# Kernel tuning notes

Hardware: AMD Instinct MI355X
Metric: run time of the kernel (lower is better)

Reference implementation:

```python
import jax, jax.numpy as jnp
import numpy as np

# SemiConv2d with semifield_type='MaxMin':
#   out[n,oc,i,j] = max_{ic,kh,kw} min(x_pad[n,ic,i+kh,j+kw], kernel[oc,ic,kh,kw])
# stride=1, 'same' padding with -inf (identity of max).

def setup_inputs() -> dict:
    key = jax.random.key(0)
    kx, kk = jax.random.split(key)
    x = jax.random.normal(kx, (8, 32, 96, 96), dtype=jnp.float32)
    kernel = jax.random.normal(kk, (32, 32, 3, 3), dtype=jnp.float32)
    return {"x": x, "kernel": kernel}


def reference(x, kernel):
    N, IC, H, W = x.shape
    OC, IC2, KH, KW = kernel.shape
    assert IC == IC2
    # same padding for k=3, stride=1 (left=top=1, right=bottom=1)
    p = KH - 1
    top = left = p // 2
    bot = right = p - top
    xp = jnp.pad(x, ((0, 0), (0, 0), (top, bot), (left, right)),
                 constant_values=-jnp.inf)
    out = None
    # small fixed loop over kernel taps (KH*KW = 9); vectorized over N, OC, IC, H, W
    for kh in range(KH):
        for kw in range(KW):
            win = xp[:, :, kh:kh + H, kw:kw + W]           # [N, IC, H, W]
            k_tap = kernel[:, :, kh, kw]                   # [OC, IC]
            # min over values, max over input channels -> [N, OC, H, W]
            v = jnp.max(jnp.minimum(win[:, None], k_tap[None, :, :, None, None]), axis=2)
            out = v if out is None else jnp.maximum(out, v)
    return out
```

## Files before the change

### kernel.cpp

```cpp
#include <hip/hip_runtime.h>
#include <math.h>


#define HH 96
#define WW 96
#define CIN 32
#define OCN 32
#define XQ_ROWS 98
#define XQ_W 48
#define XQ_SLICE (XQ_ROWS * XQ_W)
#define XQ_TOTAL (256 * XQ_SLICE)
#define K2_TOTAL (8 * 32 * 4 * 9)
#define WS_NEED ((size_t)XQ_TOTAL * 8 + (size_t)K2_TOTAL * 4)
#define NEGH2 0xFC00FC00u

typedef _Float16 h2 __attribute__((ext_vector_type(2)));

__device__ __forceinline__ uint32_t pkmin_vs(uint32_t x, uint32_t k) {
    uint32_t d;
    asm("v_pk_min_f16 %0, %1, %2" : "=v"(d) : "v"(x), "s"(k));
    return d;
}
__device__ __forceinline__ uint32_t pkmax(uint32_t a, uint32_t b) {
    uint32_t d;
    asm("v_pk_max_f16 %0, %1, %2" : "=v"(d) : "v"(a), "v"(b));
    return d;
}

__global__ __launch_bounds__(256) void setup_xq(const float* __restrict__ x,
                                                uint2* __restrict__ xq) {
    int idx = blockIdx.x * 256 + threadIdx.x;
    int j  = idx % XQ_W;
    int t  = idx / XQ_W;
    int hp = t % XQ_ROWS;
    int s  = t / XQ_ROWS;
    int h  = hp - 1;
    bool hv = (h >= 0) && (h < HH);
    const float* row = x + ((size_t)s * HH + (hv ? h : 0)) * WW;
    float a = (hv && j > 0)        ? row[2 * j - 1] : -INFINITY;
    float b = hv                   ? row[2 * j]     : -INFINITY;
    float c = hv                   ? row[2 * j + 1] : -INFINITY;
    float d = (hv && j < XQ_W - 1) ? row[2 * j + 2] : -INFINITY;
    h2 p0 = {(_Float16)a, (_Float16)b};
    h2 p1 = {(_Float16)c, (_Float16)d};
    uint2 v;
    v.x = __builtin_bit_cast(uint32_t, p0);
    v.y = __builtin_bit_cast(uint32_t, p1);
    xq[idx] = v;
}

__global__ __launch_bounds__(256) void setup_k(const float* __restrict__ kk,
                                               uint32_t* __restrict__ k2) {
    int idx = blockIdx.x * 256 + threadIdx.x;
    int tap  = idx % 9;
    int ocin = (idx / 9) % 4;
    int ic   = (idx / 36) % CIN;
    int ocb  = idx / (36 * CIN);
    float v = kk[(((ocb * 4 + ocin) * CIN) + ic) * 9 + tap];
    _Float16 hv = (_Float16)v;
    h2 p = {hv, hv};
    k2[idx] = __builtin_bit_cast(uint32_t, p);
}

__global__ __launch_bounds__(192) void semiconv_f16(const uint2* __restrict__ xq,
                                                    const uint32_t* __restrict__ k2,
                                                    float* __restrict__ out) {
    const int tid = threadIdx.x;
    const int jj = tid % 48;
    const int hr = tid / 48;
    const int b  = blockIdx.x;
    const int hp  = b % 24;
    const int t   = b / 24;
    const int ocb = t & 7;
    const int n   = t >> 3;
    const int h   = hp * 4 + hr;

    const uint2* p = xq + ((size_t)(n * CIN) * XQ_ROWS + h) * XQ_W + jj;
    const uint32_t* kp = k2 + (size_t)ocb * CIN * 36;

    uint32_t acc[4] = {NEGH2, NEGH2, NEGH2, NEGH2};

    for (int ic0 = 0; ic0 < CIN; ic0 += 2) {
        uint2 q[2][3];
#pragma unroll
        for (int u = 0; u < 2; ++u)
#pragma unroll
            for (int r = 0; r < 3; ++r)
                q[u][r] = p[u * XQ_SLICE + r * XQ_W];

#pragma unroll
        for (int u = 0; u < 2; ++u) {
            uint32_t tap[9];
#pragma unroll
            for (int r = 0; r < 3; ++r) {
                tap[r * 3 + 0] = q[u][r].x;
                tap[r * 3 + 1] = __builtin_amdgcn_alignbit(q[u][r].y, q[u][r].x, 16);
                tap[r * 3 + 2] = q[u][r].y;
            }
            const uint32_t* kq0 = kp + (ic0 + u) * 36;
#pragma unroll
            for (int oc = 0; oc < 4; ++oc) {
                const uint32_t* kq = kq0 + oc * 9;
                uint32_t m0 = pkmin_vs(tap[0], kq[0]);
                uint32_t m1 = pkmin_vs(tap[1], kq[1]);
                uint32_t m2 = pkmin_vs(tap[2], kq[2]);
                uint32_t m3 = pkmin_vs(tap[3], kq[3]);
                uint32_t m4 = pkmin_vs(tap[4], kq[4]);
                uint32_t m5 = pkmin_vs(tap[5], kq[5]);
                uint32_t m6 = pkmin_vs(tap[6], kq[6]);
                uint32_t m7 = pkmin_vs(tap[7], kq[7]);
                uint32_t m8 = pkmin_vs(tap[8], kq[8]);
                uint32_t t01 = pkmax(m0, m1), t23 = pkmax(m2, m3);
                uint32_t t45 = pkmax(m4, m5), t67 = pkmax(m6, m7);
                uint32_t tt  = pkmax(pkmax(t01, t23), pkmax(t45, t67));
                acc[oc] = pkmax(acc[oc], pkmax(tt, m8));
            }
        }
        p += 2 * XQ_SLICE;
    }

#pragma unroll
    for (int oc = 0; oc < 4; ++oc) {
        h2 a = __builtin_bit_cast(h2, acc[oc]);
        float2 v = make_float2((float)a.x, (float)a.y);
        *(float2*)(out + (((size_t)(n * OCN + ocb * 4 + oc)) * HH + h) * WW + 2 * jj) = v;
    }
}

#define NEGINF (-INFINITY)
__global__ __launch_bounds__(192, 8) void semiconv2d_f32(
    const float* __restrict__ x, const float* __restrict__ kk, float* __restrict__ out)
{
    const int tid = threadIdx.x;
    const int w  = tid % WW;
    const int hr = tid / WW;
    const int b   = blockIdx.x;
    const int ocb = b & 7;
    const int hp  = (b >> 3) % 48;
    const int n   = (b >> 3) / 48;
    const int h   = hp * 2 + hr;
    const int oc0 = ocb * 4;
    float a0[4], a1[4], a2[4];
#pragma unroll
    for (int i = 0; i < 4; ++i) { a0[i] = NEGINF; a1[i] = NEGINF; a2[i] = NEGINF; }
    const bool vm = (h > 0), vp = (h < HH - 1);
    const int hm  = vm ? h - 1 : h;
    const int hpl = vp ? h + 1 : h;
    const int cm  = (w > 0) ? -1 : 0;
    const int cp  = (w < WW - 1) ? 1 : 0;
    const float* rm = x + ((size_t)(n * CIN) * HH + hm)  * WW + w;
    const float* r1 = x + ((size_t)(n * CIN) * HH + h)   * WW + w;
    const float* rp = x + ((size_t)(n * CIN) * HH + hpl) * WW + w;
#pragma unroll 2
    for (int ic = 0; ic < CIN; ++ic) {
        float r00 = vm ? rm[cm] : NEGINF, r01 = vm ? rm[0] : NEGINF, r02 = vm ? rm[cp] : NEGINF;
        float r10 = r1[cm], r11 = r1[0], r12 = r1[cp];
        float r20 = vp ? rp[cm] : NEGINF, r21 = vp ? rp[0] : NEGINF, r22 = vp ? rp[cp] : NEGINF;
#pragma unroll
        for (int oc = 0; oc < 4; ++oc) {
            const float* kq = kk + (size_t)(((oc0 + oc) * CIN + ic)) * 9;
            a0[oc] = fmaxf(fmaxf(a0[oc], fminf(r00, kq[0])), fmaxf(fminf(r10, kq[3]), fminf(r20, kq[6])));
            a1[oc] = fmaxf(fmaxf(a1[oc], fminf(r01, kq[1])), fmaxf(fminf(r11, kq[4]), fminf(r21, kq[7])));
            a2[oc] = fmaxf(fmaxf(a2[oc], fminf(r02, kq[2])), fmaxf(fminf(r12, kq[5]), fminf(r22, kq[8])));
        }
        rm += HH * WW; r1 += HH * WW; rp += HH * WW;
    }
#pragma unroll
    for (int oc = 0; oc < 4; ++oc) {
        float v0 = (w > 0)      ? a0[oc] : NEGINF;
        float v2 = (w < WW - 1) ? a2[oc] : NEGINF;
        out[(((size_t)(n * OCN + oc0 + oc)) * HH + h) * WW + w] = fmaxf(fmaxf(v0, a1[oc]), v2);
    }
}

extern "C" void kernel_launch(void* const* d_in, const int* in_sizes, int n_in,
                              void* d_out, int out_size, void* d_ws, size_t ws_size,
                              hipStream_t stream) {
    const float* x  = (const float*)d_in[0];
    const float* kk = (const float*)d_in[1];
    float* out      = (float*)d_out;
    if (ws_size >= WS_NEED) {
        uint2* xq    = (uint2*)d_ws;
        uint32_t* k2 = (uint32_t*)(xq + XQ_TOTAL);
        setup_xq<<<dim3(XQ_TOTAL / 256), dim3(256), 0, stream>>>(x, xq);
        setup_k<<<dim3(K2_TOTAL / 256), dim3(256), 0, stream>>>(kk, k2);
        semiconv_f16<<<dim3(8 * 8 * 24), dim3(192), 0, stream>>>(xq, k2, out);
    } else {
        semiconv2d_f32<<<dim3(8 * 48 * 8), dim3(192), 0, stream>>>(x, kk, out);
    }
}
```

Measured before the change: 102.8 us.

## Stage input tiles in LDS via direct global-to-LDS loads, two rows per thread

The f16 semiring convolution now copies 8-channel chunks of a 10-row input band into shared memory with global_load_lds, then has each thread compute two adjacent output rows. This reuses the overlapping rows of the 3x3 window from LDS instead of re-reading them from global memory, and halves the block count. The cost is extra barriers per chunk, about 30 KB of LDS per block, and a grid of 768 blocks, which may lower occupancy and latency hiding.

```diff
diff --git a/kernel.cpp b/kernel.cpp
--- a/kernel.cpp
+++ b/kernel.cpp
@@ -1,5 +1,6 @@
 #include <hip/hip_runtime.h>
 #include <math.h>
+#include <stdint.h>
 
 
 #define HH 96
@@ -15,6 +16,8 @@
 #define NEGH2 0xFC00FC00u
 
 typedef _Float16 h2 __attribute__((ext_vector_type(2)));
+typedef __attribute__((address_space(3))) uint32_t lds_u32;
+typedef const __attribute__((address_space(1))) uint32_t glb_u32;
 
 __device__ __forceinline__ uint32_t pkmin_vs(uint32_t x, uint32_t k) {
     uint32_t d;
@@ -25,6 +28,10 @@
     uint32_t d;
     asm("v_pk_max_f16 %0, %1, %2" : "=v"(d) : "v"(a), "v"(b));
     return d;
+}
+__device__ __forceinline__ uint32_t packh2(float lo, float hi) {
+    h2 p = {(_Float16)lo, (_Float16)hi};
+    return __builtin_bit_cast(uint32_t, p);
 }
 
 __global__ __launch_bounds__(256) void setup_xq(const float* __restrict__ x,
@@ -41,11 +48,9 @@
     float b = hv                   ? row[2 * j]     : -INFINITY;
     float c = hv                   ? row[2 * j + 1] : -INFINITY;
     float d = (hv && j < XQ_W - 1) ? row[2 * j + 2] : -INFINITY;
-    h2 p0 = {(_Float16)a, (_Float16)b};
-    h2 p1 = {(_Float16)c, (_Float16)d};
     uint2 v;
-    v.x = __builtin_bit_cast(uint32_t, p0);
-    v.y = __builtin_bit_cast(uint32_t, p1);
+    v.x = packh2(a, b);
+    v.y = packh2(c, d);
     xq[idx] = v;
 }
 
@@ -57,74 +62,92 @@
     int ic   = (idx / 36) % CIN;
     int ocb  = idx / (36 * CIN);
     float v = kk[(((ocb * 4 + ocin) * CIN) + ic) * 9 + tap];
-    _Float16 hv = (_Float16)v;
-    h2 p = {hv, hv};
-    k2[idx] = __builtin_bit_cast(uint32_t, p);
-}
-
-__global__ __launch_bounds__(192) void semiconv_f16(const uint2* __restrict__ xq,
-                                                    const uint32_t* __restrict__ k2,
-                                                    float* __restrict__ out) {
+    k2[idx] = packh2(v, v);
+}
+
+__global__ __launch_bounds__(192) void semiconv_f16_lds(const uint2* __restrict__ xq,
+                                                        const uint32_t* __restrict__ k2,
+                                                        float* __restrict__ out) {
+    __shared__ uint2 xls[8 * 480];
+
     const int tid = threadIdx.x;
     const int jj = tid % 48;
     const int hr = tid / 48;
     const int b  = blockIdx.x;
-    const int hp  = b % 24;
-    const int t   = b / 24;
+    const int hp  = b % 12;
+    const int t   = b / 12;
     const int ocb = t & 7;
     const int n   = t >> 3;
-    const int h   = hp * 4 + hr;
-
-    const uint2* p = xq + ((size_t)(n * CIN) * XQ_ROWS + h) * XQ_W + jj;
+    const int h0  = hp * 8;
+    const int hh  = h0 + 2 * hr;
+
     const uint32_t* kp = k2 + (size_t)ocb * CIN * 36;
 
-    uint32_t acc[4] = {NEGH2, NEGH2, NEGH2, NEGH2};
-
-    for (int ic0 = 0; ic0 < CIN; ic0 += 2) {
-        uint2 q[2][3];
-#pragma unroll
-        for (int u = 0; u < 2; ++u)
-#pragma unroll
-            for (int r = 0; r < 3; ++r)
-                q[u][r] = p[u * XQ_SLICE + r * XQ_W];
-
-#pragma unroll
-        for (int u = 0; u < 2; ++u) {
-            uint32_t tap[9];
-#pragma unroll
-            for (int r = 0; r < 3; ++r) {
-                tap[r * 3 + 0] = q[u][r].x;
-                tap[r * 3 + 1] = __builtin_amdgcn_alignbit(q[u][r].y, q[u][r].x, 16);
-                tap[r * 3 + 2] = q[u][r].y;
-            }
-            const uint32_t* kq0 = kp + (ic0 + u) * 36;
+    uint32_t acc[4][2];
+#pragma unroll
+    for (int oc = 0; oc < 4; ++oc) { acc[oc][0] = NEGH2; acc[oc][1] = NEGH2; }
+
+    const uintptr_t gbase = (uintptr_t)(xq + ((size_t)(n * CIN) * XQ_ROWS + h0) * XQ_W);
+    const uintptr_t lbase = (uintptr_t)(&xls[0]);
+    const uint32_t wave_u = (uint32_t)(tid & ~63) * 16;
+
+    for (int cc = 0; cc < 4; ++cc) {
+        __syncthreads();
+#pragma unroll
+        for (int r = 0; r < 10; ++r) {
+            int i   = r * 192 + tid;
+            int icl = i / 240;
+            int off = i % 240;
+            glb_u32* gsrc = (glb_u32*)(gbase
+                + ((size_t)(cc * 8 + icl) * XQ_SLICE) * 8 + (size_t)off * 16);
+            lds_u32* ldst = (lds_u32*)(lbase + (uint32_t)(r * 192 * 16) + wave_u);
+            __builtin_amdgcn_global_load_lds(gsrc, ldst, 16, 0, 0);
+        }
+        __syncthreads();
+
+        const uint2* xl = xls + 96 * hr + jj;
+#pragma unroll
+        for (int u = 0; u < 8; ++u) {
+            const uint2* xr = xl + u * 480;
+            uint2 w0 = xr[0], w1 = xr[48], w2 = xr[96], w3 = xr[144];
+            uint32_t xt[4][3];
+            xt[0][0] = w0.x; xt[0][1] = __builtin_amdgcn_alignbit(w0.y, w0.x, 16); xt[0][2] = w0.y;
+            xt[1][0] = w1.x; xt[1][1] = __builtin_amdgcn_alignbit(w1.y, w1.x, 16); xt[1][2] = w1.y;
+            xt[2][0] = w2.x; xt[2][1] = __builtin_amdgcn_alignbit(w2.y, w2.x, 16); xt[2][2] = w2.y;
+            xt[3][0] = w3.x; xt[3][1] = __builtin_amdgcn_alignbit(w3.y, w3.x, 16); xt[3][2] = w3.y;
+
+            const uint32_t* kq0 = kp + (cc * 8 + u) * 36;
 #pragma unroll
             for (int oc = 0; oc < 4; ++oc) {
                 const uint32_t* kq = kq0 + oc * 9;
-                uint32_t m0 = pkmin_vs(tap[0], kq[0]);
-                uint32_t m1 = pkmin_vs(tap[1], kq[1]);
-                uint32_t m2 = pkmin_vs(tap[2], kq[2]);
-                uint32_t m3 = pkmin_vs(tap[3], kq[3]);
-                uint32_t m4 = pkmin_vs(tap[4], kq[4]);
-                uint32_t m5 = pkmin_vs(tap[5], kq[5]);
-                uint32_t m6 = pkmin_vs(tap[6], kq[6]);
-                uint32_t m7 = pkmin_vs(tap[7], kq[7]);
-                uint32_t m8 = pkmin_vs(tap[8], kq[8]);
-                uint32_t t01 = pkmax(m0, m1), t23 = pkmax(m2, m3);
-                uint32_t t45 = pkmax(m4, m5), t67 = pkmax(m6, m7);
-                uint32_t tt  = pkmax(pkmax(t01, t23), pkmax(t45, t67));
-                acc[oc] = pkmax(acc[oc], pkmax(tt, m8));
+#pragma unroll
+                for (int o = 0; o < 2; ++o) {
+                    uint32_t m0 = pkmin_vs(xt[o][0],     kq[0]);
+                    uint32_t m1 = pkmin_vs(xt[o][1],     kq[1]);
+                    uint32_t m2 = pkmin_vs(xt[o][2],     kq[2]);
+                    uint32_t m3 = pkmin_vs(xt[o + 1][0], kq[3]);
+                    uint32_t m4 = pkmin_vs(xt[o + 1][1], kq[4]);
+                    uint32_t m5 = pkmin_vs(xt[o + 1][2], kq[5]);
+                    uint32_t m6 = pkmin_vs(xt[o + 2][0], kq[6]);
+                    uint32_t m7 = pkmin_vs(xt[o + 2][1], kq[7]);
+                    uint32_t m8 = pkmin_vs(xt[o + 2][2], kq[8]);
+                    uint32_t t01 = pkmax(m0, m1), t23 = pkmax(m2, m3);
+                    uint32_t t45 = pkmax(m4, m5), t67 = pkmax(m6, m7);
+                    uint32_t tt  = pkmax(pkmax(t01, t23), pkmax(t45, t67));
+                    acc[oc][o] = pkmax(acc[oc][o], pkmax(tt, m8));
+                }
             }
         }
-        p += 2 * XQ_SLICE;
-    }
-
-#pragma unroll
-    for (int oc = 0; oc < 4; ++oc) {
-        h2 a = __builtin_bit_cast(h2, acc[oc]);
-        float2 v = make_float2((float)a.x, (float)a.y);
-        *(float2*)(out + (((size_t)(n * OCN + ocb * 4 + oc)) * HH + h) * WW + 2 * jj) = v;
-    }
+    }
+
+#pragma unroll
+    for (int oc = 0; oc < 4; ++oc)
+#pragma unroll
+        for (int o = 0; o < 2; ++o) {
+            h2 a = __builtin_bit_cast(h2, acc[oc][o]);
+            float2 v = make_float2((float)a.x, (float)a.y);
+            *(float2*)(out + (((size_t)(n * OCN + ocb * 4 + oc)) * HH + hh + o) * WW + 2 * jj) = v;
+        }
 }
 
 #define NEGINF (-INFINITY)
@@ -184,7 +207,7 @@
         uint32_t* k2 = (uint32_t*)(xq + XQ_TOTAL);
         setup_xq<<<dim3(XQ_TOTAL / 256), dim3(256), 0, stream>>>(x, xq);
         setup_k<<<dim3(K2_TOTAL / 256), dim3(256), 0, stream>>>(kk, k2);
-        semiconv_f16<<<dim3(8 * 8 * 24), dim3(192), 0, stream>>>(xq, k2, out);
+        semiconv_f16_lds<<<dim3(8 * 8 * 12), dim3(192), 0, stream>>>(xq, k2, out);
     } else {
         semiconv2d_f32<<<dim3(8 * 48 * 8), dim3(192), 0, stream>>>(x, kk, out);
     }
```

New measurement: 105.9 us. +3.1%, slower.
